# Optimization experiments

Measured on AMD Instinct MI355X. Metric: run time of the kernel, lower is better.

Reference implementation:

```python
import jax, jax.numpy as jnp
import numpy as np

B, T, C = 2, 2048, 1024
LAT = 256
N_HEAD = 16
HEAD_DIM = C // N_HEAD
SCALE = 1.0 / np.sqrt(HEAD_DIM).astype(np.float32)


def setup_inputs() -> dict:
    key = jax.random.key(0)
    ks = jax.random.split(key, 9)
    s_in = 0.02  # small init so softmax is well-conditioned
    return {
        "x": jax.random.normal(ks[0], (B, T, C), dtype=jnp.float32),
        "wq_lat": jax.random.normal(ks[1], (C, LAT), dtype=jnp.float32) * s_in,
        "wk_lat": jax.random.normal(ks[2], (C, LAT), dtype=jnp.float32) * s_in,
        "wv_lat": jax.random.normal(ks[3], (C, LAT), dtype=jnp.float32) * s_in,
        "wq_heads": jax.random.normal(ks[4], (LAT, C), dtype=jnp.float32) * s_in,
        "wk_heads": jax.random.normal(ks[5], (LAT, C), dtype=jnp.float32) * s_in,
        "wv_heads": jax.random.normal(ks[6], (LAT, C), dtype=jnp.float32) * s_in,
        "w_proj": jax.random.normal(ks[7], (C, C), dtype=jnp.float32) * s_in,
        "b_proj": jnp.zeros((C,), dtype=jnp.float32),
    }


def reference(x, wq_lat, wk_lat, wv_lat, wq_heads, wk_heads, wv_heads, w_proj, b_proj):
    Bx, Tx, Cx = x.shape
    # low-rank latent projections then up-projection to per-head q/k/v
    q = (x @ wq_lat) @ wq_heads  # [B,T,C]
    k = (x @ wk_lat) @ wk_heads
    v = (x @ wv_lat) @ wv_heads
    q = q.reshape(Bx, Tx, N_HEAD, HEAD_DIM).transpose(0, 2, 1, 3)  # [B,H,T,D]
    k = k.reshape(Bx, Tx, N_HEAD, HEAD_DIM).transpose(0, 2, 1, 3)
    v = v.reshape(Bx, Tx, N_HEAD, HEAD_DIM).transpose(0, 2, 1, 3)
    att = jnp.einsum("bhqd,bhkd->bhqk", q, k) * SCALE  # [B,H,T,T]
    causal = jnp.tril(jnp.ones((Tx, Tx), dtype=bool))
    att = jnp.where(causal[None, None], att, -jnp.inf)
    att = jax.nn.softmax(att, axis=-1)
    y = jnp.einsum("bhqk,bhkd->bhqd", att, v)  # [B,H,T,D]
    y = y.transpose(0, 2, 1, 3).reshape(Bx, Tx, Cx)
    return y @ w_proj + b_proj
```

## Files before the change

kernel.cpp:

```cpp
#include <hip/hip_runtime.h>

#define SCALE 0.125f
#define SL 0.18033688011112042f

typedef __bf16 bf16x8 __attribute__((ext_vector_type(8)));
typedef short short4v __attribute__((ext_vector_type(4)));
typedef unsigned short u16x4 __attribute__((ext_vector_type(4)));
typedef float f32x4 __attribute__((ext_vector_type(4)));
typedef unsigned int uint2v __attribute__((ext_vector_type(2)));

__device__ __forceinline__ unsigned short f2b(float f) {
  unsigned u = __float_as_uint(f);
  u += 0x7fffu + ((u >> 16) & 1u);
  return (unsigned short)(u >> 16);
}
__device__ __forceinline__ float ex2(float x) {
  float r;
  asm("v_exp_f32 %0, %1" : "=v"(r) : "v"(x));
  return r;
}

#define GLB(p) ((__attribute__((address_space(1))) void*)(void*)(p))
#define LDSP(p) ((__attribute__((address_space(3))) void*)(p))

__global__ __launch_bounds__(256) void prep(
    const float* __restrict__ x, const float* __restrict__ wq_lat,
    const float* __restrict__ wk_lat, const float* __restrict__ wv_lat,
    const float* __restrict__ wq_h, const float* __restrict__ wk_h,
    const float* __restrict__ wv_h, const float* __restrict__ w_proj,
    unsigned short* __restrict__ x_bf, unsigned short* __restrict__ wlatT,
    unsigned short* __restrict__ whT, unsigned short* __restrict__ wpT) {
  __shared__ float tile[32][33];
  const int blk = blockIdx.x, tid = threadIdx.x;
  if (blk < 1024) {
    int i = blk * 256 + tid;
#pragma unroll
    for (int j = 0; j < 4; j++) {
      float4 v = ((const float4*)x)[i + j * 262144];
      u16x4 p;
      p.x = f2b(v.x); p.y = f2b(v.y); p.z = f2b(v.z); p.w = f2b(v.w);
      ((u16x4*)x_bf)[i + j * 262144] = p;
    }
  } else if (blk < 1792) {
    int idx = blk - 1024;
    int z = idx >> 8, rem = idx & 255;
    const float* wsrc = z == 0 ? wq_lat : (z == 1 ? wk_lat : wv_lat);
    unsigned short* o = wlatT + z * 262144;
    int c0 = (rem & 7) * 32, r0 = (rem >> 3) * 32;
    int tx = tid & 31, ty = tid >> 5;
#pragma unroll
    for (int i = 0; i < 32; i += 8) tile[ty + i][tx] = wsrc[(r0 + ty + i) * 256 + c0 + tx];
    __syncthreads();
#pragma unroll
    for (int i = 0; i < 32; i += 8) o[(c0 + ty + i) * 1024 + r0 + tx] = f2b(tile[tx][ty + i]);
  } else if (blk < 2560) {
    int idx = blk - 1792;
    int z = idx >> 8, rem = idx & 255;
    const float* wsrc = z == 0 ? wq_h : (z == 1 ? wk_h : wv_h);
    unsigned short* o = whT + z * 262144;
    int c0 = (rem & 31) * 32, r0 = (rem >> 5) * 32;
    int tx = tid & 31, ty = tid >> 5;
#pragma unroll
    for (int i = 0; i < 32; i += 8) tile[ty + i][tx] = wsrc[(r0 + ty + i) * 1024 + c0 + tx];
    __syncthreads();
#pragma unroll
    for (int i = 0; i < 32; i += 8) o[(c0 + ty + i) * 256 + r0 + tx] = f2b(tile[tx][ty + i]);
  } else {
    int idx = blk - 2560;
    int c0 = (idx & 31) * 32, r0 = (idx >> 5) * 32;
    int tx = tid & 31, ty = tid >> 5;
#pragma unroll
    for (int i = 0; i < 32; i += 8) tile[ty + i][tx] = w_proj[(r0 + ty + i) * 1024 + c0 + tx];
    __syncthreads();
#pragma unroll
    for (int i = 0; i < 32; i += 8) wpT[(c0 + ty + i) * 1024 + r0 + tx] = f2b(tile[tx][ty + i]);
  }
}

template <int MODE>
__global__ __launch_bounds__(256) void gemm_bt(
    const unsigned short* __restrict__ A0, const unsigned short* __restrict__ A1,
    const unsigned short* __restrict__ A2,
    const unsigned short* __restrict__ B0, const unsigned short* __restrict__ B1,
    const unsigned short* __restrict__ B2,
    void* __restrict__ C0, void* __restrict__ C1, void* __restrict__ C2,
    const float* __restrict__ bias, int M, int N, int K) {
  const int z = blockIdx.z;
  const unsigned short* A = z == 0 ? A0 : (z == 1 ? A1 : A2);
  const unsigned short* BT = z == 0 ? B0 : (z == 1 ? B1 : B2);
  void* C = z == 0 ? C0 : (z == 1 ? C1 : C2);

  __shared__ char smem[32768];

  const int t = threadIdx.x;
  const int n0 = blockIdx.x * 128;
  const int m0 = blockIdx.y * 128;
  const int lane = t & 63;
  const int wid = t >> 6;
  const int wr = wid >> 1, wc = wid & 1;
  const int lo = lane & 15, g = lane >> 4;

  f32x4 acc[4][4];
#pragma unroll
  for (int i = 0; i < 4; i++)
#pragma unroll
    for (int j = 0; j < 4; j++) acc[i][j] = (f32x4){0.f, 0.f, 0.f, 0.f};

  const unsigned short* ga = A + (size_t)(m0 + (t >> 2)) * K + (t & 3) * 8;
  const unsigned short* gb = BT + (size_t)(n0 + (t >> 2)) * K + (t & 3) * 8;
  const size_t rowK64 = (size_t)64 * K;
  char* dA = smem + t * 16;
  char* dB = smem + 16384 + t * 16;
  const char* rA = smem + (wr * 64 + lo) * 64 + g * 16;
  const char* rB = smem + 16384 + (wc * 64 + lo) * 64 + g * 16;

#define STGB(D, kof)                                                                     \
  __builtin_amdgcn_global_load_lds(GLB(ga + (kof)), LDSP(dA + (D)*8192), 16, 0, 0);      \
  __builtin_amdgcn_global_load_lds(GLB(ga + rowK64 + (kof)), LDSP(dA + (D)*8192 + 4096), 16, 0, 0); \
  __builtin_amdgcn_global_load_lds(GLB(gb + (kof)), LDSP(dB + (D)*8192), 16, 0, 0);      \
  __builtin_amdgcn_global_load_lds(GLB(gb + rowK64 + (kof)), LDSP(dB + (D)*8192 + 4096), 16, 0, 0);

#define COMPB(D)                                                                         \
  {                                                                                      \
    bf16x8 af[4], bfr[4];                                                                \
    _Pragma("unroll") for (int i = 0; i < 4; i++) {                                      \
      af[i] = *(const bf16x8*)(rA + (D)*8192 + i * 1024);                                \
      bfr[i] = *(const bf16x8*)(rB + (D)*8192 + i * 1024);                               \
    }                                                                                    \
    __builtin_amdgcn_s_setprio(1);                                                       \
    _Pragma("unroll") for (int i = 0; i < 4; i++)                                        \
    _Pragma("unroll") for (int j = 0; j < 4; j++)                                        \
        acc[i][j] = __builtin_amdgcn_mfma_f32_16x16x32_bf16(af[i], bfr[j], acc[i][j], 0, 0, 0); \
    __builtin_amdgcn_s_setprio(0);                                                       \
  }

  STGB(0, 0);
  asm volatile("s_waitcnt vmcnt(0)" ::: "memory");
  __builtin_amdgcn_s_barrier();
  for (int k0 = 0; k0 < K; k0 += 64) {
    if (k0 + 32 < K) { STGB(1, k0 + 32); }
    COMPB(0);
    asm volatile("s_waitcnt vmcnt(0)" ::: "memory");
    __builtin_amdgcn_s_barrier();
    if (k0 + 64 < K) { STGB(0, k0 + 64); }
    COMPB(1);
    asm volatile("s_waitcnt vmcnt(0)" ::: "memory");
    __builtin_amdgcn_s_barrier();
  }
#undef STGB
#undef COMPB

  if constexpr (MODE == 2) {
    float* Cf = (float*)C;
#pragma unroll
    for (int i = 0; i < 4; i++) {
      int row0 = m0 + wr * 64 + i * 16 + g * 4;
#pragma unroll
      for (int j = 0; j < 4; j++) {
        int col = n0 + wc * 64 + j * 16 + lo;
        float bv = bias[col];
#pragma unroll
        for (int r = 0; r < 4; r++) Cf[(size_t)(row0 + r) * N + col] = acc[i][j][r] + bv;
      }
    }
  } else {
    unsigned short* Cb = (unsigned short*)C;
#pragma unroll
    for (int i = 0; i < 4; i++) {
      int row0 = m0 + wr * 64 + i * 16 + g * 4;
#pragma unroll
      for (int j = 0; j < 4; j++) {
        int col = n0 + wc * 64 + j * 16 + lo;
#pragma unroll
        for (int r = 0; r < 4; r++) Cb[(size_t)(row0 + r) * N + col] = f2b(acc[i][j][r]);
      }
    }
  }
}

__global__ __launch_bounds__(512) void gemm_up8(const unsigned short* __restrict__ A,
                                                const unsigned short* __restrict__ BT,
                                                unsigned short* __restrict__ Qo,
                                                unsigned short* __restrict__ Ko,
                                                unsigned short* __restrict__ Vo) {
  __shared__ char smem[131072];

  const int t = threadIdx.x;
  const int lane = t & 63;
  const int wid = t >> 6;
  const int wr = wid >> 2, wc = wid & 3;
  const int lo = lane & 15, g = lane >> 4;
  const int lin = blockIdx.x;
  const int xcd = lin & 7;
  const int slot = lin >> 3;
  const int by = (xcd << 1) | (slot >= 12 ? 1 : 0);
  const int bx = slot >= 12 ? slot - 12 : slot;
  const int m0 = by * 256;
  const int z = bx >> 2;
  const int ncb = (bx & 3) * 256;
  const unsigned short* Az = A + (size_t)z * 1048576;
  const unsigned short* Bz = BT + (size_t)z * 262144;

  const int slog8 = (((t & 3) ^ ((t >> 2) & 3) ^ (((t >> 4) & 1) << 1)) << 3);
  const unsigned short *aS00, *aS01, *aS10, *aS11, *bS00, *bS01, *bS10, *bS11;
  {
    const int r = t >> 2;
    aS00 = Az + (size_t)(m0 + r) * 256 + slog8;
    aS01 = Az + (size_t)(m0 + r + 128) * 256 + slog8;
    aS10 = aS00 + 32;
    aS11 = aS01 + 32;
    bS00 = Bz + (size_t)(ncb + r) * 256 + slog8;
    bS01 = Bz + (size_t)(ncb + r + 128) * 256 + slog8;
    bS10 = bS00 + 32;
    bS11 = bS01 + 32;
  }
  char* dA0 = smem + t * 16;
  char* dA1 = smem + 16384 + t * 16;
  char* dB0 = smem + 32768 + t * 16;
  char* dB1 = smem + 49152 + t * 16;

  const int slotA = ((g ^ (lo & 3) ^ (((lo >> 2) & 1) << 1)) << 4);
  const char* aR = smem + (wr * 128 + lo) * 64 + slotA;
  const char* bR = smem + 32768 + (wc * 64 + lo) * 64 + slotA;

  f32x4 acc[8][4];
#pragma unroll
  for (int i = 0; i < 8; i++)
#pragma unroll
    for (int j = 0; j < 4; j++) acc[i][j] = (f32x4){0.f, 0.f, 0.f, 0.f};

#define STG(p0, p1, dst, D)                                                              \
  __builtin_amdgcn_global_load_lds(GLB(p0), LDSP(dst + (D)*65536), 16, 0, 0);            \
  __builtin_amdgcn_global_load_lds(GLB(p1), LDSP(dst + (D)*65536 + 8192), 16, 0, 0);     \
  p0 += 64; p1 += 64;

#define MF16(FRB, af, bf)                                                                \
  __builtin_amdgcn_s_setprio(1);                                                         \
  _Pragma("unroll") for (int i = 0; i < 4; i++)                                          \
  _Pragma("unroll") for (int j = 0; j < 4; j++)                                          \
      acc[(FRB) + i][j] = __builtin_amdgcn_mfma_f32_16x16x32_bf16(af[i], bf[j],          \
                                                                  acc[(FRB) + i][j], 0, 0, 0); \
  __builtin_amdgcn_s_setprio(0);

#define TILE(D, S)                                                                       \
  {                                                                                      \
    bf16x8 af[4], bf[4];                                                                 \
    _Pragma("unroll") for (int j = 0; j < 4; j++)                                        \
        bf[j] = *(const bf16x8*)(bR + (D)*65536 + j * 1024);                             \
    _Pragma("unroll") for (int i = 0; i < 4; i++)                                        \
        af[i] = *(const bf16x8*)(aR + (D)*65536 + i * 1024);                             \
    if (S) { STG(aS00, aS01, dA0, (D) ^ 1); }                                            \
    __builtin_amdgcn_s_barrier();                                                        \
    MF16(0, af, bf);                                                                     \
    __builtin_amdgcn_s_barrier();                                                        \
    _Pragma("unroll") for (int i = 0; i < 4; i++)                                        \
        af[i] = *(const bf16x8*)(aR + (D)*65536 + (4 + i) * 1024);                       \
    if (S) { STG(bS00, bS01, dB0, (D) ^ 1); }                                            \
    __builtin_amdgcn_s_barrier();                                                        \
    MF16(4, af, bf);                                                                     \
    if (S) { asm volatile("s_waitcnt vmcnt(4)" ::: "memory"); }                          \
    else   { asm volatile("s_waitcnt vmcnt(0)" ::: "memory"); }                          \
    __builtin_amdgcn_s_barrier();                                                        \
    _Pragma("unroll") for (int j = 0; j < 4; j++)                                        \
        bf[j] = *(const bf16x8*)(bR + (D)*65536 + 16384 + j * 1024);                     \
    _Pragma("unroll") for (int i = 0; i < 4; i++)                                        \
        af[i] = *(const bf16x8*)(aR + (D)*65536 + 16384 + i * 1024);                     \
    if (S) { STG(aS10, aS11, dA1, (D) ^ 1); }                                            \
    __builtin_amdgcn_s_barrier();                                                        \
    MF16(0, af, bf);                                                                     \
    __builtin_amdgcn_s_barrier();                                                        \
    _Pragma("unroll") for (int i = 0; i < 4; i++)                                        \
        af[i] = *(const bf16x8*)(aR + (D)*65536 + 16384 + (4 + i) * 1024);               \
    if (S) { STG(bS10, bS11, dB1, (D) ^ 1); }                                            \
    __builtin_amdgcn_s_barrier();                                                        \
    MF16(4, af, bf);                                                                     \
    if (S) { asm volatile("s_waitcnt vmcnt(4)" ::: "memory"); }                          \
    __builtin_amdgcn_s_barrier();                                                        \
  }

  { STG(aS00, aS01, dA0, 0); }
  { STG(bS00, bS01, dB0, 0); }
  { STG(aS10, aS11, dA1, 0); }
  { STG(bS10, bS11, dB1, 0); }
  asm volatile("s_waitcnt vmcnt(0)" ::: "memory");
  __builtin_amdgcn_s_barrier();

  TILE(0, 1);
  TILE(1, 1);
  TILE(0, 1);
  TILE(1, 0);

#undef TILE
#undef MF16
#undef STG

  if (z < 2) {
    unsigned short* Cb = z == 0 ? Qo : Ko;
    const float scl = z == 0 ? SL : 1.0f;
#pragma unroll
    for (int fr = 0; fr < 8; fr++) {
      int row0 = m0 + wr * 128 + fr * 16 + g * 4;
#pragma unroll
      for (int fc = 0; fc < 4; fc++) {
        int col = ncb + wc * 64 + fc * 16 + lo;
#pragma unroll
        for (int r = 0; r < 4; r++) Cb[(size_t)(row0 + r) * 1024 + col] = f2b(acc[fr][fc][r] * scl);
      }
    }
  } else {
#pragma unroll
    for (int fr = 0; fr < 8; fr++) {
      int row0 = m0 + wr * 128 + fr * 16 + g * 4;
      int bb = row0 >> 11, tloc = row0 & 2047;
#pragma unroll
      for (int fc = 0; fc < 4; fc++) {
        int col = ncb + wc * 64 + fc * 16 + lo;
        u16x4 pk;
#pragma unroll
        for (int r = 0; r < 4; r++) pk[r] = f2b(acc[fr][fc][r]);
        *(u16x4*)&Vo[((size_t)(bb * 1024) + col) * 2048 + tloc] = pk;
      }
    }
  }
}

__global__ __launch_bounds__(256) void attn_fwd(const unsigned short* __restrict__ Q,
                                                const unsigned short* __restrict__ K,
                                                const unsigned short* __restrict__ VT,
                                                unsigned short* __restrict__ Y) {
  __shared__ char smem[32768];

  const int tid = threadIdx.x;
  const int w = tid >> 6;
  const int lane = tid & 63;
  const int lo = lane & 15, g = lane >> 4;
  const int lo7 = lo & 7;
  const int bid = blockIdx.x;
  const int bh = bid & 31;
  const int code = bid >> 5;
  const int qq = code >> 3, kk = code & 7;
  const int chunk = qq == 0 ? 31 - kk : (qq == 1 ? 16 + kk : (qq == 2 ? 15 - kk : kk));
  const int b = bh >> 4, h = bh & 15;
  const int q0 = chunk * 64 + w * 16;

  const unsigned short* Qb = Q + (size_t)(b * 2048) * 1024 + h * 64;
  const unsigned short* Kb = K + (size_t)(b * 2048) * 1024 + h * 64;
  const unsigned short* Vb = VT + (size_t)((b * 16 + h) * 64) * 2048;

  bf16x8 qf0 = *(const bf16x8*)(Qb + (size_t)(q0 + lo) * 1024 + g * 8);
  bf16x8 qf1 = *(const bf16x8*)(Qb + (size_t)(q0 + lo) * 1024 + 32 + g * 8);

  const f32x4 z4 = (f32x4){0.f, 0.f, 0.f, 0.f};
  f32x4 acc[4];
#pragma unroll
  for (int dt = 0; dt < 4; dt++) acc[dt] = z4;
  float lrun = 0.f;
  const int nt = chunk + 1;

  const int koff = lo * 128 + ((g ^ lo7) << 4);
  char* kb0 = smem + koff;
  char* kb1 = smem + (koff ^ 64);
  const int voff = lo * 128 + ((g ^ ((lo7 & 1) << 1)) << 3) + ((lo7 >> 1) << 5);
  char* vq0 = smem + 16384 + voff;
  char* vq1 = smem + 16384 + (voff ^ 32);
  char* vq2 = smem + 16384 + (voff ^ 64);
  char* vq3 = smem + 16384 + (voff ^ 96);

  const int r0s = tid >> 3, c0s = (tid & 7) ^ (r0s & 7);
  const unsigned short* sk0 = Kb + (size_t)r0s * 1024 + c0s * 8;
  const unsigned short* sk1 = sk0 + (size_t)32 * 1024;
  const unsigned short* sv0 = Vb + (size_t)r0s * 2048 + c0s * 8;
  const unsigned short* sv1 = sv0 + (size_t)32 * 2048;
  char* dk0 = smem + tid * 16;
  char* dk1 = smem + 4096 + tid * 16;
  char* dv0 = smem + 16384 + tid * 16;
  char* dv1 = smem + 20480 + tid * 16;

#define STAGE(BUF)                                                                        \
  __builtin_amdgcn_global_load_lds(GLB(sk0), LDSP(dk0 + (BUF)*8192), 16, 0, 0);           \
  __builtin_amdgcn_global_load_lds(GLB(sk1), LDSP(dk1 + (BUF)*8192), 16, 0, 0);           \
  __builtin_amdgcn_global_load_lds(GLB(sv0), LDSP(dv0 + (BUF)*8192), 16, 0, 0);           \
  __builtin_amdgcn_global_load_lds(GLB(sv1), LDSP(dv1 + (BUF)*8192), 16, 0, 0);           \
  sk0 += 65536; sk1 += 65536; sv0 += 64; sv1 += 64;

#define COMPUTE(k0v, BUF, MASKED)                                                         \
  {                                                                                       \
    bf16x8 kfA[4], kfB[4];                                                                \
    _Pragma("unroll") for (int kvf = 0; kvf < 4; kvf++) {                                 \
      kfA[kvf] = *(const bf16x8*)(kb0 + (BUF)*8192 + kvf * 2048);                         \
      kfB[kvf] = *(const bf16x8*)(kb1 + (BUF)*8192 + kvf * 2048);                         \
    }                                                                                     \
    short4v vf[4][4];                                                                     \
    _Pragma("unroll") for (int kvf = 0; kvf < 4; kvf++) {                                 \
      const char* vp = kvf == 0 ? vq0 : (kvf == 1 ? vq1 : (kvf == 2 ? vq2 : vq3));        \
      _Pragma("unroll") for (int dt = 0; dt < 4; dt++)                                    \
          vf[dt][kvf] = *(const short4v*)(vp + (BUF)*8192 + dt * 2048);                   \
    }                                                                                     \
    f32x4 st[4];                                                                          \
    __builtin_amdgcn_s_setprio(1);                                                        \
    _Pragma("unroll") for (int kvf = 0; kvf < 4; kvf++) {                                 \
      st[kvf] = __builtin_amdgcn_mfma_f32_16x16x32_bf16(kfA[kvf], qf0, z4, 0, 0, 0);      \
      st[kvf] = __builtin_amdgcn_mfma_f32_16x16x32_bf16(kfB[kvf], qf1, st[kvf], 0, 0, 0); \
    }                                                                                     \
    __builtin_amdgcn_s_setprio(0);                                                        \
    if (MASKED) {                                                                         \
      const int qg = q0 + lo;                                                             \
      _Pragma("unroll") for (int kvf = 0; kvf < 4; kvf++)                                 \
      _Pragma("unroll") for (int r = 0; r < 4; r++) {                                     \
        int tk = (k0v) + kvf * 16 + g * 4 + r;                                            \
        if (tk > qg) st[kvf][r] = -3.0e38f;                                               \
      }                                                                                   \
    }                                                                                     \
    __builtin_amdgcn_s_setprio(1);                                                        \
    _Pragma("unroll") for (int kvf = 0; kvf < 4; kvf++) {                                 \
      float p0 = ex2(st[kvf][0]);                                                         \
      float p1 = ex2(st[kvf][1]);                                                         \
      float p2 = ex2(st[kvf][2]);                                                         \
      float p3 = ex2(st[kvf][3]);                                                         \
      lrun += (p0 + p1) + (p2 + p3);                                                      \
      uint2v pw;                                                                          \
      pw.x = __builtin_amdgcn_perm(__float_as_uint(p1), __float_as_uint(p0), 0x07060302u); \
      pw.y = __builtin_amdgcn_perm(__float_as_uint(p3), __float_as_uint(p2), 0x07060302u); \
      short4v pb = __builtin_bit_cast(short4v, pw);                                       \
      _Pragma("unroll") for (int dt = 0; dt < 4; dt++)                                    \
          acc[dt] = __builtin_amdgcn_mfma_f32_16x16x16bf16_1k(vf[dt][kvf], pb,            \
                                                              acc[dt], 0, 0, 0);          \
    }                                                                                     \
    __builtin_amdgcn_s_setprio(0);                                                        \
  }

  STAGE(0);
  __syncthreads();
  int t = 0;
  for (; t + 2 <= nt - 1; t += 2) {
    STAGE(1);
    COMPUTE(t * 64, 0, false);
    __syncthreads();
    STAGE(0);
    COMPUTE(t * 64 + 64, 1, false);
    __syncthreads();
  }
  if (t < nt - 1) {
    STAGE(1);
    COMPUTE(t * 64, 0, false);
    __syncthreads();
    COMPUTE(t * 64 + 64, 1, true);
  } else {
    COMPUTE(t * 64, 0, true);
  }

  {
    float l = lrun;
    l += __shfl_xor(l, 16);
    l += __shfl_xor(l, 32);
    float inv = 1.0f / l;
    unsigned short* yp = Y + (size_t)(b * 2048 + q0 + lo) * 1024 + h * 64;
#pragma unroll
    for (int dt = 0; dt < 4; dt++) {
      float y0 = acc[dt][0] * inv, y1 = acc[dt][1] * inv;
      float y2 = acc[dt][2] * inv, y3 = acc[dt][3] * inv;
      uint2v pw;
      pw.x = __builtin_amdgcn_perm(__float_as_uint(y1), __float_as_uint(y0), 0x07060302u);
      pw.y = __builtin_amdgcn_perm(__float_as_uint(y3), __float_as_uint(y2), 0x07060302u);
      *(uint2v*)&yp[dt * 16 + g * 4] = pw;
    }
  }
#undef STAGE
#undef COMPUTE
}

extern "C" void kernel_launch(void* const* d_in, const int* in_sizes, int n_in,
                              void* d_out, int out_size, void* d_ws, size_t ws_size,
                              hipStream_t stream) {
  const float* x = (const float*)d_in[0];
  const float* wq_lat = (const float*)d_in[1];
  const float* wk_lat = (const float*)d_in[2];
  const float* wv_lat = (const float*)d_in[3];
  const float* wq_h = (const float*)d_in[4];
  const float* wk_h = (const float*)d_in[5];
  const float* wv_h = (const float*)d_in[6];
  const float* w_proj = (const float*)d_in[7];
  const float* b_proj = (const float*)d_in[8];
  float* out = (float*)d_out;

  char* ws = (char*)d_ws;
  unsigned short* x_bf = (unsigned short*)(ws + 0);
  unsigned short* wlatT = (unsigned short*)(ws + 8388608);
  unsigned short* whT = (unsigned short*)(ws + 9961472);
  unsigned short* wpT = (unsigned short*)(ws + 11534336);
  unsigned short* lat = (unsigned short*)(ws + 13631488);
  unsigned short* q_bf = (unsigned short*)(ws + 19922944);
  unsigned short* k_bf = (unsigned short*)(ws + 28311552);
  unsigned short* vT = (unsigned short*)(ws + 36700160);
  unsigned short* y_bf = (unsigned short*)(ws + 45088768);

  prep<<<3584, 256, 0, stream>>>(x, wq_lat, wk_lat, wv_lat, wq_h, wk_h, wv_h, w_proj,
                                 x_bf, wlatT, whT, wpT);

  gemm_bt<0><<<dim3(2, 32, 3), 256, 0, stream>>>(
      x_bf, x_bf, x_bf, wlatT, wlatT + 262144, wlatT + 524288,
      lat, lat + 1048576, lat + 2097152, nullptr, 4096, 256, 1024);

  gemm_up8<<<192, 512, 0, stream>>>(lat, whT, q_bf, k_bf, vT);

  attn_fwd<<<1024, 256, 0, stream>>>(q_bf, k_bf, vT, y_bf);

  gemm_bt<2><<<dim3(8, 32, 1), 256, 0, stream>>>(
      y_bf, y_bf, y_bf, wpT, wpT, wpT, out, out, out, b_proj, 4096, 1024, 1024);
}
```

Before: 98.56 us.

## Split long causal attention rows across two blocks with a combine pass

The upper half of query chunks (16-31) now has its key range split into two halves, each handled by a separate block that writes unnormalized fp32 partial accumulators and row sums into reused workspace regions. A new combine kernel adds the two partials, normalizes and writes bf16 output. The aim is to balance the causal workload and raise the block count from 1024 to 1536 so the GPU is filled better. The cost is an extra launch plus fp32 partial traffic. The split works without a running max because the softmax omits max subtraction, which relies on the small input scale.

```diff
diff --git a/kernel.cpp b/kernel.cpp
--- a/kernel.cpp
+++ b/kernel.cpp
@@ -327,7 +327,10 @@
 __global__ __launch_bounds__(256) void attn_fwd(const unsigned short* __restrict__ Q,
                                                 const unsigned short* __restrict__ K,
                                                 const unsigned short* __restrict__ VT,
-                                                unsigned short* __restrict__ Y) {
+                                                unsigned short* __restrict__ Y,
+                                                float* __restrict__ pwsA,
+                                                float* __restrict__ pwsB,
+                                                float* __restrict__ plr) {
   __shared__ char smem[32768];
 
   const int tid = threadIdx.x;
@@ -338,8 +341,20 @@
   const int bid = blockIdx.x;
   const int bh = bid & 31;
   const int code = bid >> 5;
-  const int qq = code >> 3, kk = code & 7;
-  const int chunk = qq == 0 ? 31 - kk : (qq == 1 ? 16 + kk : (qq == 2 ? 15 - kk : kk));
+  int chunk, ts, ntile, pidx = 0;
+  if (code < 32) {
+    chunk = 31 - (code >> 1);
+    const int half = code & 1;
+    const int h0 = (chunk + 2) >> 1;
+    ts = half ? h0 : 0;
+    ntile = half ? (chunk + 1 - h0) : h0;
+    pidx = ((bh * 16 + (chunk - 16)) * 2 + half);
+  } else {
+    chunk = 47 - code;
+    ts = 0;
+    ntile = chunk + 1;
+  }
+  const bool split = (code < 32);
   const int b = bh >> 4, h = bh & 15;
   const int q0 = chunk * 64 + w * 16;
 
@@ -355,7 +370,6 @@
 #pragma unroll
   for (int dt = 0; dt < 4; dt++) acc[dt] = z4;
   float lrun = 0.f;
-  const int nt = chunk + 1;
 
   const int koff = lo * 128 + ((g ^ lo7) << 4);
   char* kb0 = smem + koff;
@@ -367,9 +381,9 @@
   char* vq3 = smem + 16384 + (voff ^ 96);
 
   const int r0s = tid >> 3, c0s = (tid & 7) ^ (r0s & 7);
-  const unsigned short* sk0 = Kb + (size_t)r0s * 1024 + c0s * 8;
+  const unsigned short* sk0 = Kb + (size_t)(ts * 64 + r0s) * 1024 + c0s * 8;
   const unsigned short* sk1 = sk0 + (size_t)32 * 1024;
-  const unsigned short* sv0 = Vb + (size_t)r0s * 2048 + c0s * 8;
+  const unsigned short* sv0 = Vb + (size_t)r0s * 2048 + ts * 64 + c0s * 8;
   const unsigned short* sv1 = sv0 + (size_t)32 * 2048;
   char* dk0 = smem + tid * 16;
   char* dk1 = smem + 4096 + tid * 16;
@@ -432,41 +446,80 @@
   STAGE(0);
   __syncthreads();
   int t = 0;
-  for (; t + 2 <= nt - 1; t += 2) {
+  for (; t + 2 <= ntile - 1; t += 2) {
     STAGE(1);
-    COMPUTE(t * 64, 0, false);
+    COMPUTE((ts + t) * 64, 0, false);
     __syncthreads();
     STAGE(0);
-    COMPUTE(t * 64 + 64, 1, false);
+    COMPUTE((ts + t + 1) * 64, 1, false);
     __syncthreads();
   }
-  if (t < nt - 1) {
+  if (t < ntile - 1) {
     STAGE(1);
-    COMPUTE(t * 64, 0, false);
+    COMPUTE((ts + t) * 64, 0, false);
     __syncthreads();
-    COMPUTE(t * 64 + 64, 1, true);
+    COMPUTE((ts + t + 1) * 64, 1, true);
   } else {
-    COMPUTE(t * 64, 0, true);
+    COMPUTE((ts + t) * 64, 0, true);
   }
 
   {
     float l = lrun;
     l += __shfl_xor(l, 16);
     l += __shfl_xor(l, 32);
-    float inv = 1.0f / l;
-    unsigned short* yp = Y + (size_t)(b * 2048 + q0 + lo) * 1024 + h * 64;
-#pragma unroll
-    for (int dt = 0; dt < 4; dt++) {
-      float y0 = acc[dt][0] * inv, y1 = acc[dt][1] * inv;
-      float y2 = acc[dt][2] * inv, y3 = acc[dt][3] * inv;
-      uint2v pw;
-      pw.x = __builtin_amdgcn_perm(__float_as_uint(y1), __float_as_uint(y0), 0x07060302u);
-      pw.y = __builtin_amdgcn_perm(__float_as_uint(y3), __float_as_uint(y2), 0x07060302u);
-      *(uint2v*)&yp[dt * 16 + g * 4] = pw;
+    if (split) {
+      float* base = pidx < 704 ? pwsA + (size_t)pidx * 4096
+                               : pwsB + (size_t)(pidx - 704) * 4096;
+      float* pp = base + (size_t)(w * 16 + lo) * 64;
+#pragma unroll
+      for (int dt = 0; dt < 4; dt++) *(f32x4*)&pp[dt * 16 + g * 4] = acc[dt];
+      if (g == 0) plr[pidx * 64 + w * 16 + lo] = l;
+    } else {
+      float inv = 1.0f / l;
+      unsigned short* yp = Y + (size_t)(b * 2048 + q0 + lo) * 1024 + h * 64;
+#pragma unroll
+      for (int dt = 0; dt < 4; dt++) {
+        float y0 = acc[dt][0] * inv, y1 = acc[dt][1] * inv;
+        float y2 = acc[dt][2] * inv, y3 = acc[dt][3] * inv;
+        uint2v pw;
+        pw.x = __builtin_amdgcn_perm(__float_as_uint(y1), __float_as_uint(y0), 0x07060302u);
+        pw.y = __builtin_amdgcn_perm(__float_as_uint(y3), __float_as_uint(y2), 0x07060302u);
+        *(uint2v*)&yp[dt * 16 + g * 4] = pw;
+      }
     }
   }
 #undef STAGE
 #undef COMPUTE
+}
+
+__global__ __launch_bounds__(256) void attn_comb(const float* __restrict__ pwsA,
+                                                 const float* __restrict__ pwsB,
+                                                 const float* __restrict__ plr,
+                                                 unsigned short* __restrict__ Y) {
+  const int blk = blockIdx.x;
+  const int bh = blk >> 4, ci = blk & 15;
+  const int b = bh >> 4, h = bh & 15;
+  const int c = 16 + ci;
+  const int tid = threadIdx.x;
+  const int q = tid >> 2, d0 = (tid & 3) * 16;
+  const int pi0 = blk * 2, pi1 = blk * 2 + 1;
+  const float* base0 = pi0 < 704 ? pwsA + (size_t)pi0 * 4096 : pwsB + (size_t)(pi0 - 704) * 4096;
+  const float* base1 = pi1 < 704 ? pwsA + (size_t)pi1 * 4096 : pwsB + (size_t)(pi1 - 704) * 4096;
+  const float* p0 = base0 + (size_t)q * 64 + d0;
+  const float* p1 = base1 + (size_t)q * 64 + d0;
+  const float inv = 1.0f / (plr[pi0 * 64 + q] + plr[pi1 * 64 + q]);
+  unsigned short* yp = Y + (size_t)(b * 2048 + c * 64 + q) * 1024 + h * 64 + d0;
+#pragma unroll
+  for (int i = 0; i < 4; i++) {
+    f32x4 a = *(const f32x4*)&p0[i * 4];
+    f32x4 bb = *(const f32x4*)&p1[i * 4];
+    float y0 = (a[0] + bb[0]) * inv, y1 = (a[1] + bb[1]) * inv;
+    float y2 = (a[2] + bb[2]) * inv, y3 = (a[3] + bb[3]) * inv;
+    uint2v pw;
+    pw.x = __builtin_amdgcn_perm(__float_as_uint(y1), __float_as_uint(y0), 0x07060302u);
+    pw.y = __builtin_amdgcn_perm(__float_as_uint(y3), __float_as_uint(y2), 0x07060302u);
+    *(uint2v*)&yp[i * 4] = pw;
+  }
 }
 
 extern "C" void kernel_launch(void* const* d_in, const int* in_sizes, int n_in,
@@ -493,6 +546,9 @@
   unsigned short* k_bf = (unsigned short*)(ws + 28311552);
   unsigned short* vT = (unsigned short*)(ws + 36700160);
   unsigned short* y_bf = (unsigned short*)(ws + 45088768);
+  float* pwsA = (float*)(ws + 0);
+  float* pwsB = (float*)(ws + 13631488);
+  float* plr = (float*)(ws + 18874368);
 
   prep<<<3584, 256, 0, stream>>>(x, wq_lat, wk_lat, wv_lat, wq_h, wk_h, wv_h, w_proj,
                                  x_bf, wlatT, whT, wpT);
@@ -503,7 +559,8 @@
 
   gemm_up8<<<192, 512, 0, stream>>>(lat, whT, q_bf, k_bf, vT);
 
-  attn_fwd<<<1024, 256, 0, stream>>>(q_bf, k_bf, vT, y_bf);
+  attn_fwd<<<1536, 256, 0, stream>>>(q_bf, k_bf, vT, y_bf, pwsA, pwsB, plr);
+  attn_comb<<<512, 256, 0, stream>>>(pwsA, pwsB, plr, y_bf);
 
   gemm_bt<2><<<dim3(8, 32, 1), 256, 0, stream>>>(
       y_bf, y_bf, y_bf, wpT, wpT, wpT, out, out, out, b_proj, 4096, 1024, 1024);
```

New measurement: 104.4 us. +6.0%, slower.
